# Kernel tuning notes

Measured on AMD Instinct MI355X. Metric: run time of the kernel, lower is better.

Reference implementation:

```python
import jax, jax.numpy as jnp
import numpy as np

B, N, D, H, HD = 1, 2048, 1024, 16, 64
INNER = H * HD
WINDOW_RATIO = 0.125  # docstring default in _create_window_mask


def rotate_half(x):
    # interleaved pair rotation: (x0,x1) -> (-x1,x0), per x-transformers
    pairs = x.reshape(x.shape[:-1] + (-1, 2))
    x1, x2 = pairs[..., 0], pairs[..., 1]
    return jnp.stack([-x2, x1], axis=-1).reshape(x.shape)


def apply_rope(t, freqs):
    # rotate only the first rot_dim channels, pass the rest through
    rot = freqs.shape[-1]
    t_rot, t_pass = t[..., :rot], t[..., rot:]
    t_rot = t_rot * jnp.cos(freqs) + rotate_half(t_rot) * jnp.sin(freqs)
    return jnp.concatenate([t_rot, t_pass], axis=-1)


def setup_inputs() -> dict:
    key = jax.random.key(0)
    ks = jax.random.split(key, 12)
    x = jax.random.normal(ks[0], (B, N, D), jnp.float32)
    mask = jnp.ones((B, N), dtype=bool)
    # rotary freqs of width dim_head (x-transformers style, repeated r=2)
    pos = jnp.arange(N, dtype=jnp.float32)
    inv = 1.0 / (10000.0 ** (jnp.arange(0, HD, 2, dtype=jnp.float32) / HD))
    freqs = jnp.repeat(pos[:, None] * inv[None, :], 2, axis=-1)  # [N, HD]
    s = 0.02
    Wq = jax.random.normal(ks[1], (D, INNER), jnp.float32) * s
    bq = jax.random.normal(ks[2], (INNER,), jnp.float32) * s
    Wk = jax.random.normal(ks[3], (D, INNER), jnp.float32) * s
    bk = jax.random.normal(ks[4], (INNER,), jnp.float32) * s
    Wv = jax.random.normal(ks[5], (D, INNER), jnp.float32) * s
    bv = jax.random.normal(ks[6], (INNER,), jnp.float32) * s
    Wo = jax.random.normal(ks[7], (INNER, D), jnp.float32) * s
    bo = jax.random.normal(ks[8], (D,), jnp.float32) * s
    return {"x": x, "mask": mask, "freqs": freqs, "Wq": Wq, "bq": bq,
            "Wk": Wk, "bk": bk, "Wv": Wv, "bv": bv, "Wo": Wo, "bo": bo}


def reference(x, mask, freqs, Wq, bq, Wk, bk, Wv, bv, Wo, bo):
    b, n, _ = x.shape
    q = apply_rope(x @ Wq + bq, freqs)  # q_xpos_scale = 1.0
    k = apply_rope(x @ Wk + bk, freqs)  # k_xpos_scale = 1.0
    v = x @ Wv + bv
    # [b,n,inner] -> [b,h,n,hd]
    q = q.reshape(b, n, H, HD).transpose(0, 2, 1, 3)
    k = k.reshape(b, n, H, HD).transpose(0, 2, 1, 3)
    v = v.reshape(b, n, H, HD).transpose(0, 2, 1, 3)
    scale = 1.0 / jnp.sqrt(jnp.asarray(HD, q.dtype))
    scores = jnp.einsum('bhqd,bhkd->bhqk', q, k) * scale  # computed once, reused
    # sliding-window mask: row i attends [i-ws//2, i+ws//2] inclusive
    ws = int(n * WINDOW_RATIO)
    i = jnp.arange(n)[:, None]
    j = jnp.arange(n)[None, :]
    wmask = (j >= i - ws // 2) & (j <= i + ws // 2)  # [n,n]
    keymask = mask[:, None, None, :]  # [b,1,1,n]
    NEG = jnp.asarray(-1e9, scores.dtype)
    full_p = jax.nn.softmax(jnp.where(keymask, scores, NEG), axis=-1)
    win_p = jax.nn.softmax(jnp.where(wmask[None, None] & keymask, scores, NEG), axis=-1)
    full_attn = jnp.einsum('bhqk,bhkd->bhqd', full_p, v)
    win_attn = jnp.einsum('bhqk,bhkd->bhqd', win_p, v)
    window_residual = full_attn - win_attn  # [b,h,n,hd]
    out = full_attn.transpose(0, 2, 1, 3).reshape(b, n, INNER) @ Wo + bo
    out = jnp.where(mask[..., None], out, jnp.asarray(0.0, out.dtype))
    return (out, window_residual)
```

## Files before the change

### kernel.cpp

```cpp
#include <hip/hip_runtime.h>
#include <cstdint>

#define SEQ 2048
#define DM 1024
#define NH 16
#define HD 64

typedef short s8v __attribute__((ext_vector_type(8)));
typedef float f4v __attribute__((ext_vector_type(4)));

__device__ __forceinline__ short f2bf(float x) {
  union { float f; unsigned u; } v; v.f = x;
  return (short)((v.u + 0x7fffu + ((v.u >> 16) & 1u)) >> 16);
}

__device__ __forceinline__ void load_lds16(const void* g, void* l) {
  auto gp = reinterpret_cast<const __attribute__((address_space(1))) unsigned int*>(
      reinterpret_cast<uintptr_t>(g));
  auto lp = reinterpret_cast<__attribute__((address_space(3))) unsigned int*>(
      reinterpret_cast<uintptr_t>(l));
  __builtin_amdgcn_global_load_lds(gp, lp, 16, 0, 0);
}

__global__ __launch_bounds__(256) void convert_x_kernel(const float* __restrict__ x,
                                                        short* __restrict__ xb) {
  int i = blockIdx.x * 256 + threadIdx.x;
  float4 v = ((const float4*)x)[i];
  short4 o;
  o.x = f2bf(v.x); o.y = f2bf(v.y); o.z = f2bf(v.z); o.w = f2bf(v.w);
  ((short4*)xb)[i] = o;
}

__global__ __launch_bounds__(256) void transpose_w_kernel(
    const float* __restrict__ W0, const float* __restrict__ W1,
    const float* __restrict__ W2, const float* __restrict__ W3,
    short* __restrict__ T0, short* __restrict__ T1,
    short* __restrict__ T2, short* __restrict__ T3) {
  const float* W; short* T;
  switch (blockIdx.z) {
    case 0: W = W0; T = T0; break;
    case 1: W = W1; T = T1; break;
    case 2: W = W2; T = T2; break;
    default: W = W3; T = T3; break;
  }
  __shared__ float tile[32][33];
  int tx = threadIdx.x, ty = threadIdx.y;
  int bc = blockIdx.x * 32, br = blockIdx.y * 32;
#pragma unroll
  for (int i = 0; i < 4; ++i)
    tile[ty + i * 8][tx] = W[(size_t)(br + ty + i * 8) * DM + bc + tx];
  __syncthreads();
#pragma unroll
  for (int i = 0; i < 4; ++i)
    T[(size_t)(bc + ty + i * 8) * DM + br + tx] = f2bf(tile[tx][ty + i * 8]);
}

template <int BM, int BN>
__device__ __forceinline__ void gemm_body(const short* __restrict__ A,
                                          const short* __restrict__ BT,
                                          const float* __restrict__ bias,
                                          const float* __restrict__ freqs,
                                          short* __restrict__ ob, float* __restrict__ of,
                                          int mode, short* At, short* Bt) {
  const int tid = threadIdx.x;
  const int wave = tid >> 6, lane = tid & 63;
  const int quad = lane >> 4, l16 = lane & 15;
  const int m0 = blockIdx.x * BM, n0 = blockIdx.y * BN;
  const int wm = (wave & 1) * (BM / 2), wn = (wave >> 1) * (BN / 2);
  constexpr int MI = BM / 32, NI = BN / 32;

  f4v acc[MI][NI];
  f4v zero = {0.f, 0.f, 0.f, 0.f};
#pragma unroll
  for (int i = 0; i < MI; ++i)
#pragma unroll
    for (int j = 0; j < NI; ++j) acc[i][j] = zero;

  for (int k0 = 0; k0 < DM; k0 += 32) {
#pragma unroll
    for (int i = 0; i < BM / 64; ++i) {
      int e = (tid + i * 256) * 8;
      int row = e >> 5, col = e & 31;
      load_lds16(A + (size_t)(m0 + row) * DM + k0 + col, At + (wave * 64 + i * 256) * 8);
    }
#pragma unroll
    for (int i = 0; i < BN / 64; ++i) {
      int e = (tid + i * 256) * 8;
      int row = e >> 5, col = e & 31;
      load_lds16(BT + (size_t)(n0 + row) * DM + k0 + col, Bt + (wave * 64 + i * 256) * 8);
    }
    __syncthreads();
    s8v a[MI], b[NI];
#pragma unroll
    for (int mi = 0; mi < MI; ++mi)
      a[mi] = *(const s8v*)(At + (wm + mi * 16 + l16) * 32 + quad * 8);
#pragma unroll
    for (int ni = 0; ni < NI; ++ni)
      b[ni] = *(const s8v*)(Bt + (wn + ni * 16 + l16) * 32 + quad * 8);
#pragma unroll
    for (int mi = 0; mi < MI; ++mi)
#pragma unroll
      for (int ni = 0; ni < NI; ++ni)
        acc[mi][ni] = __builtin_amdgcn_mfma_f32_16x16x32_bf16(a[mi], b[ni], acc[mi][ni], 0, 0, 0);
    __syncthreads();
  }

#pragma unroll
  for (int mi = 0; mi < MI; ++mi) {
#pragma unroll
    for (int ni = 0; ni < NI; ++ni) {
      const int col = n0 + wn + ni * 16 + l16;
      const float bv = bias[col];
      const int row0 = m0 + wm + mi * 16 + quad * 4;
      if (mode == 2) {
        short4 o;
        o.x = f2bf(acc[mi][ni][0] + bv);
        o.y = f2bf(acc[mi][ni][1] + bv);
        o.z = f2bf(acc[mi][ni][2] + bv);
        o.w = f2bf(acc[mi][ni][3] + bv);
        *(short4*)(ob + (size_t)col * SEQ + row0) = o;
      } else if (mode == 3) {
#pragma unroll
        for (int r = 0; r < 4; ++r)
          of[(size_t)(row0 + r) * DM + col] = acc[mi][ni][r] + bv;
      } else {
#pragma unroll
        for (int r = 0; r < 4; ++r) {
          const int row = row0 + r;
          float v = acc[mi][ni][r] + bv;
          if (col < HD) {
            float f = freqs[row * HD + col];
            float partner = __shfl_xor(v, 1);
            float cs = cosf(f), sn = sinf(f);
            v = v * cs + ((col & 1) ? partner : -partner) * sn;
          }
          ob[(size_t)(col >> 6) * (SEQ * HD) + (size_t)row * HD + (col & 63)] = f2bf(v);
        }
      }
    }
  }
}

__global__ __launch_bounds__(256) void gemm_qkv_kernel(
    const short* __restrict__ A, const short* __restrict__ BTq,
    const short* __restrict__ BTk, const short* __restrict__ BTv,
    const float* __restrict__ bq, const float* __restrict__ bk,
    const float* __restrict__ bv, const float* __restrict__ freqs,
    short* __restrict__ q, short* __restrict__ k, short* __restrict__ v) {
  __shared__ __align__(16) short At[64 * 32];
  __shared__ __align__(16) short Bt[128 * 32];
  const int z = blockIdx.z;
  const short* BT = z == 0 ? BTq : (z == 1 ? BTk : BTv);
  const float* bias = z == 0 ? bq : (z == 1 ? bk : bv);
  short* ob = z == 0 ? q : (z == 1 ? k : v);
  gemm_body<64, 128>(A, BT, bias, freqs, ob, nullptr, z, At, Bt);
}

__global__ __launch_bounds__(256) void gemm_o_kernel(const short* __restrict__ A,
                                                     const short* __restrict__ BT,
                                                     const float* __restrict__ bias,
                                                     float* __restrict__ of) {
  __shared__ __align__(16) short At[64 * 32];
  __shared__ __align__(16) short Bt[64 * 32];
  gemm_body<64, 64>(A, BT, bias, nullptr, nullptr, of, 3, At, Bt);
}


__device__ __forceinline__ void online_update2(const f4v sf[4], float& m, float& l,
                                               f4v O[4], short* pw, const short* vlds,
                                               int quad, int l16) {
  float mx = -3.0e38f;
#pragma unroll
  for (int nt = 0; nt < 4; ++nt)
#pragma unroll
    for (int r = 0; r < 4; ++r) mx = fmaxf(mx, sf[nt][r]);
  mx = fmaxf(mx, __shfl_xor(mx, 16));
  mx = fmaxf(mx, __shfl_xor(mx, 32));
  const float mn = fmaxf(m, mx);
  const float alpha = exp2f(m - mn);
  m = mn;
  float s = 0.f;
  unsigned pk[4][2];
#pragma unroll
  for (int nt = 0; nt < 4; ++nt) {
    float p0 = exp2f(sf[nt][0] - mn), p1 = exp2f(sf[nt][1] - mn);
    float p2 = exp2f(sf[nt][2] - mn), p3 = exp2f(sf[nt][3] - mn);
    s += (p0 + p1) + (p2 + p3);
    pk[nt][0] = ((unsigned)(unsigned short)f2bf(p1) << 16) | (unsigned short)f2bf(p0);
    pk[nt][1] = ((unsigned)(unsigned short)f2bf(p3) << 16) | (unsigned short)f2bf(p2);
  }
  s += __shfl_xor(s, 16);
  s += __shfl_xor(s, 32);
  l = l * alpha + s;
#pragma unroll
  for (int ni = 0; ni < 4; ++ni) O[ni] *= alpha;

  const int sw = l16 & 7;
#pragma unroll
  for (int nt = 0; nt < 4; ++nt) {
    uint2 w; w.x = pk[nt][0]; w.y = pk[nt][1];
    *(uint2*)(pw + l16 * 64 + (((nt * 2 + (quad >> 1)) ^ sw) << 3) + ((quad & 1) << 2)) = w;
  }
  __builtin_amdgcn_s_waitcnt(0xC07F);
  __builtin_amdgcn_wave_barrier();
  s8v bp0 = *(const s8v*)(pw + l16 * 64 + ((quad ^ sw) << 3));
  s8v bp1 = *(const s8v*)(pw + l16 * 64 + (((4 + quad) ^ sw) << 3));
#pragma unroll
  for (int ni = 0; ni < 4; ++ni) {
    const int d = ni * 16 + l16;
    const short* vr = vlds + d * 64;
    s8v va = *(const s8v*)(vr + ((quad ^ sw) << 3));
    s8v vb = *(const s8v*)(vr + (((4 + quad) ^ sw) << 3));
    O[ni] = __builtin_amdgcn_mfma_f32_16x16x32_bf16(va, bp0, O[ni], 0, 0, 0);
    O[ni] = __builtin_amdgcn_mfma_f32_16x16x32_bf16(vb, bp1, O[ni], 0, 0, 0);
  }
  __builtin_amdgcn_wave_barrier();
}

__global__ __launch_bounds__(256, 2) void attn_kernel(const short* __restrict__ qh,
                                                      const short* __restrict__ kh,
                                                      const short* __restrict__ vT,
                                                      float* __restrict__ resid,
                                                      short* __restrict__ aws) {
  __shared__ __align__(16) short Kd[2][64 * 64];
  __shared__ __align__(16) short Vd[2][64 * 64];
  __shared__ __align__(16) short Pl[4][16 * 64];
  const int tid = threadIdx.x, wave = tid >> 6, lane = tid & 63;
  const int quad = lane >> 4, l16 = lane & 15;
  const int h = blockIdx.y;
  const int q0w = blockIdx.x * 64 + wave * 16;

  const short* kbase = kh + (size_t)h * (SEQ * HD);
  const short* vbase = vT + (size_t)h * (HD * SEQ);
  short* pw = &Pl[wave][0];

  const short* qb = qh + (size_t)h * (SEQ * HD) + (size_t)(q0w + l16) * HD;
  s8v bq0 = *(const s8v*)(qb + quad * 8);
  s8v bq1 = *(const s8v*)(qb + 32 + quad * 8);

  f4v Of[4], Ow[4];
  float mf = -3.0e38f, lf = 0.f, mw = -3.0e38f, lw = 0.f;
  f4v zero = {0.f, 0.f, 0.f, 0.f};
#pragma unroll
  for (int i = 0; i < 4; ++i) { Of[i] = zero; Ow[i] = zero; }

  const float SCALE = 0.125f * 1.44269504089f;

#pragma unroll
  for (int i = 0; i < 2; ++i) {
    const int G = wave * 64 + i * 256 + lane;
    const int r = G >> 3, gc = (G & 7) ^ (r & 7);
    load_lds16(kbase + (size_t)r * HD + gc * 8, &Kd[0][(wave * 64 + i * 256) * 8]);
    load_lds16(vbase + (size_t)r * SEQ + gc * 8, &Vd[0][(wave * 64 + i * 256) * 8]);
  }
  __syncthreads();

  for (int it = 0; it < 32; ++it) {
    const int kb = it * 64, cur = it & 1;
    if (it + 1 < 32) {
      const int kb2 = kb + 64;
#pragma unroll
      for (int i = 0; i < 2; ++i) {
        const int G = wave * 64 + i * 256 + lane;
        const int r = G >> 3, gc = (G & 7) ^ (r & 7);
        load_lds16(kbase + (size_t)(kb2 + r) * HD + gc * 8,
                   &Kd[cur ^ 1][(wave * 64 + i * 256) * 8]);
        load_lds16(vbase + (size_t)r * SEQ + kb2 + gc * 8,
                   &Vd[cur ^ 1][(wave * 64 + i * 256) * 8]);
      }
    }

    f4v sf[4];
#pragma unroll
    for (int nt = 0; nt < 4; ++nt) {
      const int j = nt * 16 + l16;
      const short* kr = &Kd[cur][j * 64];
      s8v ka = *(const s8v*)(kr + ((quad ^ (j & 7)) << 3));
      s8v kc = *(const s8v*)(kr + (((4 + quad) ^ (j & 7)) << 3));
      f4v s = zero;
      s = __builtin_amdgcn_mfma_f32_16x16x32_bf16(ka, bq0, s, 0, 0, 0);
      s = __builtin_amdgcn_mfma_f32_16x16x32_bf16(kc, bq1, s, 0, 0, 0);
      sf[nt] = s * SCALE;
    }

    online_update2(sf, mf, lf, Of, pw, &Vd[cur][0], quad, l16);

    const bool band = (kb + 63 >= q0w - 128) && (kb <= q0w + 15 + 128);
    if (band) {
      f4v swv[4];
#pragma unroll
      for (int nt = 0; nt < 4; ++nt)
#pragma unroll
        for (int r = 0; r < 4; ++r) {
          const int df = (kb + nt * 16 + quad * 4 + r) - (q0w + l16);
          swv[nt][r] = (df >= -128 && df <= 128) ? sf[nt][r] : -1.0e9f;
        }
      online_update2(swv, mw, lw, Ow, pw, &Vd[cur][0], quad, l16);
    }
    __syncthreads();
  }

  const float invf = 1.0f / lf;
  const float invw = 1.0f / lw;
  const int q = q0w + l16;
  float* rbase = resid + (size_t)h * (SEQ * HD) + (size_t)q * HD;
  short* abase = aws + (size_t)q * DM + h * HD;
#pragma unroll
  for (int ni = 0; ni < 4; ++ni) {
    const int d0 = ni * 16 + quad * 4;
    f4v fullv = Of[ni] * invf;
    f4v winv = Ow[ni] * invw;
    float4 rv;
    rv.x = fullv[0] - winv[0]; rv.y = fullv[1] - winv[1];
    rv.z = fullv[2] - winv[2]; rv.w = fullv[3] - winv[3];
    *(float4*)(rbase + d0) = rv;
    short4 o;
    o.x = f2bf(fullv[0]); o.y = f2bf(fullv[1]);
    o.z = f2bf(fullv[2]); o.w = f2bf(fullv[3]);
    *(short4*)(abase + d0) = o;
  }
}

extern "C" void kernel_launch(void* const* d_in, const int* in_sizes, int n_in,
                              void* d_out, int out_size, void* d_ws, size_t ws_size,
                              hipStream_t stream) {
  const float* x     = (const float*)d_in[0];
  const float* freqs = (const float*)d_in[2];
  const float* Wq = (const float*)d_in[3];
  const float* bq = (const float*)d_in[4];
  const float* Wk = (const float*)d_in[5];
  const float* bk = (const float*)d_in[6];
  const float* Wv = (const float*)d_in[7];
  const float* bv = (const float*)d_in[8];
  const float* Wo = (const float*)d_in[9];
  const float* bo = (const float*)d_in[10];
  float* out = (float*)d_out;

  char* ws = (char*)d_ws;
  short* Xb  = (short*)(ws);
  short* WqT = (short*)(ws + ((size_t)4  << 20));
  short* WkT = (short*)(ws + ((size_t)6  << 20));
  short* WvT = (short*)(ws + ((size_t)8  << 20));
  short* WoT = (short*)(ws + ((size_t)10 << 20));
  short* qhp = (short*)(ws + ((size_t)12 << 20));
  short* khp = (short*)(ws + ((size_t)16 << 20));
  short* vTp = (short*)(ws + ((size_t)20 << 20));
  short* aws = (short*)(ws + ((size_t)24 << 20));

  convert_x_kernel<<<SEQ * DM / 4 / 256, 256, 0, stream>>>(x, Xb);
  transpose_w_kernel<<<dim3(32, 32, 4), dim3(32, 8), 0, stream>>>(
      Wq, Wk, Wv, Wo, WqT, WkT, WvT, WoT);

  gemm_qkv_kernel<<<dim3(32, 8, 3), 256, 0, stream>>>(
      Xb, WqT, WkT, WvT, bq, bk, bv, freqs, qhp, khp, vTp);

  attn_kernel<<<dim3(32, 16), 256, 0, stream>>>(
      qhp, khp, vTp, out + (size_t)SEQ * DM, aws);

  gemm_o_kernel<<<dim3(32, 16), 256, 0, stream>>>(aws, WoT, bo, out);
}
```

Before: 202.6 us.

## Retile QKV and output GEMMs, split attention KV range across wave halves

The QKV GEMM becomes one 128x128-tile kernel with a 64-wide K step and XOR-swizzled LDS, treating the three weight matrices as one contiguous transposed buffer. It also folds the softmax scale into Q at store time. The output GEMM uses a 128-wide K step with swizzled LDS. The attention kernel now runs 512 threads, where two wave groups each handle half of the key range and their online-softmax states are merged through LDS at the end, to raise parallelism and cut the per-block serial loop. In exchange, LDS use and register pressure go up, and correctness depends on WqT/WkT/WvT being laid out contiguously in the workspace.

```diff
diff --git a/kernel.cpp b/kernel.cpp
--- a/kernel.cpp
+++ b/kernel.cpp
@@ -55,116 +55,155 @@
     T[(size_t)(bc + ty + i * 8) * DM + br + tx] = f2bf(tile[tx][ty + i * 8]);
 }
 
-template <int BM, int BN>
-__device__ __forceinline__ void gemm_body(const short* __restrict__ A,
-                                          const short* __restrict__ BT,
-                                          const float* __restrict__ bias,
-                                          const float* __restrict__ freqs,
-                                          short* __restrict__ ob, float* __restrict__ of,
-                                          int mode, short* At, short* Bt) {
-  const int tid = threadIdx.x;
-  const int wave = tid >> 6, lane = tid & 63;
+__global__ __launch_bounds__(256) void gemm_qkv_kernel(
+    const short* __restrict__ A, const short* __restrict__ BT,
+    const float* __restrict__ bqp, const float* __restrict__ bkp,
+    const float* __restrict__ bvp, const float* __restrict__ freqs,
+    short* __restrict__ q, short* __restrict__ k, short* __restrict__ v) {
+  __shared__ __align__(16) short At[128 * 64];
+  __shared__ __align__(16) short Bt[128 * 64];
+  const int tid = threadIdx.x, wave = tid >> 6, lane = tid & 63;
   const int quad = lane >> 4, l16 = lane & 15;
-  const int m0 = blockIdx.x * BM, n0 = blockIdx.y * BN;
-  const int wm = (wave & 1) * (BM / 2), wn = (wave >> 1) * (BN / 2);
-  constexpr int MI = BM / 32, NI = BN / 32;
-
-  f4v acc[MI][NI];
+  const int m0 = blockIdx.x * 128;
+  const int n0g = blockIdx.y * 128;
+  const int z = blockIdx.y >> 3;
+  const int colbase = (blockIdx.y & 7) * 128;
+  const int wm = (wave & 1) * 64, wn = (wave >> 1) * 64;
+
+  f4v acc[4][4];
   f4v zero = {0.f, 0.f, 0.f, 0.f};
 #pragma unroll
-  for (int i = 0; i < MI; ++i)
-#pragma unroll
-    for (int j = 0; j < NI; ++j) acc[i][j] = zero;
-
-  for (int k0 = 0; k0 < DM; k0 += 32) {
-#pragma unroll
-    for (int i = 0; i < BM / 64; ++i) {
-      int e = (tid + i * 256) * 8;
-      int row = e >> 5, col = e & 31;
-      load_lds16(A + (size_t)(m0 + row) * DM + k0 + col, At + (wave * 64 + i * 256) * 8);
-    }
-#pragma unroll
-    for (int i = 0; i < BN / 64; ++i) {
-      int e = (tid + i * 256) * 8;
-      int row = e >> 5, col = e & 31;
-      load_lds16(BT + (size_t)(n0 + row) * DM + k0 + col, Bt + (wave * 64 + i * 256) * 8);
+  for (int i = 0; i < 4; ++i)
+#pragma unroll
+    for (int j = 0; j < 4; ++j) acc[i][j] = zero;
+
+  for (int k0 = 0; k0 < DM; k0 += 64) {
+#pragma unroll
+    for (int i = 0; i < 4; ++i) {
+      const int G = i * 256 + tid;
+      const int r = G >> 3, gc = ((G & 7) ^ (r & 7)) << 3;
+      load_lds16(A + (size_t)(m0 + r) * DM + k0 + gc, At + G * 8);
+      load_lds16(BT + (size_t)(n0g + r) * DM + k0 + gc, Bt + G * 8);
     }
     __syncthreads();
-    s8v a[MI], b[NI];
-#pragma unroll
-    for (int mi = 0; mi < MI; ++mi)
-      a[mi] = *(const s8v*)(At + (wm + mi * 16 + l16) * 32 + quad * 8);
-#pragma unroll
-    for (int ni = 0; ni < NI; ++ni)
-      b[ni] = *(const s8v*)(Bt + (wn + ni * 16 + l16) * 32 + quad * 8);
-#pragma unroll
-    for (int mi = 0; mi < MI; ++mi)
-#pragma unroll
-      for (int ni = 0; ni < NI; ++ni)
-        acc[mi][ni] = __builtin_amdgcn_mfma_f32_16x16x32_bf16(a[mi], b[ni], acc[mi][ni], 0, 0, 0);
+#pragma unroll
+    for (int kc = 0; kc < 2; ++kc) {
+      s8v a[4], b[4];
+#pragma unroll
+      for (int mi = 0; mi < 4; ++mi) {
+        const int row = wm + mi * 16 + l16;
+        a[mi] = *(const s8v*)(At + row * 64 + (((kc * 4 + quad) ^ (row & 7)) << 3));
+      }
+#pragma unroll
+      for (int ni = 0; ni < 4; ++ni) {
+        const int row = wn + ni * 16 + l16;
+        b[ni] = *(const s8v*)(Bt + row * 64 + (((kc * 4 + quad) ^ (row & 7)) << 3));
+      }
+#pragma unroll
+      for (int mi = 0; mi < 4; ++mi)
+#pragma unroll
+        for (int ni = 0; ni < 4; ++ni)
+          acc[mi][ni] = __builtin_amdgcn_mfma_f32_16x16x32_bf16(a[mi], b[ni], acc[mi][ni], 0, 0, 0);
+    }
     __syncthreads();
   }
 
-#pragma unroll
-  for (int mi = 0; mi < MI; ++mi) {
-#pragma unroll
-    for (int ni = 0; ni < NI; ++ni) {
-      const int col = n0 + wn + ni * 16 + l16;
+  const float* bias = (z == 0) ? bqp : (z == 1) ? bkp : bvp;
+  const float SCALE = 0.125f * 1.44269504089f;
+#pragma unroll
+  for (int mi = 0; mi < 4; ++mi) {
+#pragma unroll
+    for (int ni = 0; ni < 4; ++ni) {
+      const int col = colbase + wn + ni * 16 + l16;
       const float bv = bias[col];
       const int row0 = m0 + wm + mi * 16 + quad * 4;
-      if (mode == 2) {
+      if (z == 2) {
         short4 o;
         o.x = f2bf(acc[mi][ni][0] + bv);
         o.y = f2bf(acc[mi][ni][1] + bv);
         o.z = f2bf(acc[mi][ni][2] + bv);
         o.w = f2bf(acc[mi][ni][3] + bv);
-        *(short4*)(ob + (size_t)col * SEQ + row0) = o;
-      } else if (mode == 3) {
-#pragma unroll
-        for (int r = 0; r < 4; ++r)
-          of[(size_t)(row0 + r) * DM + col] = acc[mi][ni][r] + bv;
+        *(short4*)(v + (size_t)col * SEQ + row0) = o;
       } else {
+        const bool rope = (colbase + wn) == 0;
+        short* ob = (z == 0) ? q : k;
 #pragma unroll
         for (int r = 0; r < 4; ++r) {
           const int row = row0 + r;
-          float v = acc[mi][ni][r] + bv;
-          if (col < HD) {
-            float f = freqs[row * HD + col];
-            float partner = __shfl_xor(v, 1);
-            float cs = cosf(f), sn = sinf(f);
-            v = v * cs + ((col & 1) ? partner : -partner) * sn;
+          float val = acc[mi][ni][r] + bv;
+          if (rope) {
+            const float f = freqs[row * HD + col];
+            const float partner = __shfl_xor(val, 1);
+            val = val * cosf(f) + ((col & 1) ? partner : -partner) * sinf(f);
           }
-          ob[(size_t)(col >> 6) * (SEQ * HD) + (size_t)row * HD + (col & 63)] = f2bf(v);
+          if (z == 0) val *= SCALE;
+          ob[(size_t)(col >> 6) * (SEQ * HD) + (size_t)row * HD + (col & 63)] = f2bf(val);
         }
       }
     }
   }
-}
-
-__global__ __launch_bounds__(256) void gemm_qkv_kernel(
-    const short* __restrict__ A, const short* __restrict__ BTq,
-    const short* __restrict__ BTk, const short* __restrict__ BTv,
-    const float* __restrict__ bq, const float* __restrict__ bk,
-    const float* __restrict__ bv, const float* __restrict__ freqs,
-    short* __restrict__ q, short* __restrict__ k, short* __restrict__ v) {
-  __shared__ __align__(16) short At[64 * 32];
-  __shared__ __align__(16) short Bt[128 * 32];
-  const int z = blockIdx.z;
-  const short* BT = z == 0 ? BTq : (z == 1 ? BTk : BTv);
-  const float* bias = z == 0 ? bq : (z == 1 ? bk : bv);
-  short* ob = z == 0 ? q : (z == 1 ? k : v);
-  gemm_body<64, 128>(A, BT, bias, freqs, ob, nullptr, z, At, Bt);
 }
 
 __global__ __launch_bounds__(256) void gemm_o_kernel(const short* __restrict__ A,
                                                      const short* __restrict__ BT,
                                                      const float* __restrict__ bias,
                                                      float* __restrict__ of) {
-  __shared__ __align__(16) short At[64 * 32];
-  __shared__ __align__(16) short Bt[64 * 32];
-  gemm_body<64, 64>(A, BT, bias, nullptr, nullptr, of, 3, At, Bt);
-}
-
+  __shared__ __align__(16) short At[64 * 128];
+  __shared__ __align__(16) short Bt[64 * 128];
+  const int tid = threadIdx.x, wave = tid >> 6, lane = tid & 63;
+  const int quad = lane >> 4, l16 = lane & 15;
+  const int m0 = blockIdx.x * 64, n0 = blockIdx.y * 64;
+  const int wm = (wave & 1) * 32, wn = (wave >> 1) * 32;
+
+  f4v acc[2][2];
+  f4v zero = {0.f, 0.f, 0.f, 0.f};
+#pragma unroll
+  for (int i = 0; i < 2; ++i)
+#pragma unroll
+    for (int j = 0; j < 2; ++j) acc[i][j] = zero;
+
+  for (int k0 = 0; k0 < DM; k0 += 128) {
+#pragma unroll
+    for (int i = 0; i < 4; ++i) {
+      const int G = i * 256 + tid;
+      const int r = G >> 4, gc = ((G & 15) ^ (r & 15)) << 3;
+      load_lds16(A + (size_t)(m0 + r) * DM + k0 + gc, At + G * 8);
+      load_lds16(BT + (size_t)(n0 + r) * DM + k0 + gc, Bt + G * 8);
+    }
+    __syncthreads();
+#pragma unroll
+    for (int kc = 0; kc < 4; ++kc) {
+      s8v a[2], b[2];
+#pragma unroll
+      for (int mi = 0; mi < 2; ++mi) {
+        const int row = wm + mi * 16 + l16;
+        a[mi] = *(const s8v*)(At + row * 128 + (((kc * 4 + quad) ^ (row & 15)) << 3));
+      }
+#pragma unroll
+      for (int ni = 0; ni < 2; ++ni) {
+        const int row = wn + ni * 16 + l16;
+        b[ni] = *(const s8v*)(Bt + row * 128 + (((kc * 4 + quad) ^ (row & 15)) << 3));
+      }
+#pragma unroll
+      for (int mi = 0; mi < 2; ++mi)
+#pragma unroll
+        for (int ni = 0; ni < 2; ++ni)
+          acc[mi][ni] = __builtin_amdgcn_mfma_f32_16x16x32_bf16(a[mi], b[ni], acc[mi][ni], 0, 0, 0);
+    }
+    __syncthreads();
+  }
+
+#pragma unroll
+  for (int mi = 0; mi < 2; ++mi)
+#pragma unroll
+    for (int ni = 0; ni < 2; ++ni) {
+      const int col = n0 + wn + ni * 16 + l16;
+      const float bv = bias[col];
+      const int row0 = m0 + wm + mi * 16 + quad * 4;
+#pragma unroll
+      for (int r = 0; r < 4; ++r) of[(size_t)(row0 + r) * DM + col] = acc[mi][ni][r] + bv;
+    }
+}
 
 __device__ __forceinline__ void online_update2(const f4v sf[4], float& m, float& l,
                                                f4v O[4], short* pw, const short* vlds,
@@ -207,8 +246,7 @@
   s8v bp1 = *(const s8v*)(pw + l16 * 64 + (((4 + quad) ^ sw) << 3));
 #pragma unroll
   for (int ni = 0; ni < 4; ++ni) {
-    const int d = ni * 16 + l16;
-    const short* vr = vlds + d * 64;
+    const short* vr = vlds + (ni * 16 + l16) * 64;
     s8v va = *(const s8v*)(vr + ((quad ^ sw) << 3));
     s8v vb = *(const s8v*)(vr + (((4 + quad) ^ sw) << 3));
     O[ni] = __builtin_amdgcn_mfma_f32_16x16x32_bf16(va, bp0, O[ni], 0, 0, 0);
@@ -217,18 +255,19 @@
   __builtin_amdgcn_wave_barrier();
 }
 
-__global__ __launch_bounds__(256, 2) void attn_kernel(const short* __restrict__ qh,
+__global__ __launch_bounds__(512, 4) void attn_kernel(const short* __restrict__ qh,
                                                       const short* __restrict__ kh,
                                                       const short* __restrict__ vT,
                                                       float* __restrict__ resid,
                                                       short* __restrict__ aws) {
-  __shared__ __align__(16) short Kd[2][64 * 64];
-  __shared__ __align__(16) short Vd[2][64 * 64];
-  __shared__ __align__(16) short Pl[4][16 * 64];
+  __shared__ __align__(16) short Kd[2][2][64 * 64];
+  __shared__ __align__(16) short Vd[2][2][64 * 64];
+  __shared__ __align__(16) short Pl[8][16 * 64];
   const int tid = threadIdx.x, wave = tid >> 6, lane = tid & 63;
   const int quad = lane >> 4, l16 = lane & 15;
+  const int slab = wave & 3, khalf = wave >> 2;
   const int h = blockIdx.y;
-  const int q0w = blockIdx.x * 64 + wave * 16;
+  const int q0w = blockIdx.x * 64 + slab * 16;
 
   const short* kbase = kh + (size_t)h * (SEQ * HD);
   const short* vbase = vT + (size_t)h * (HD * SEQ);
@@ -244,46 +283,37 @@
 #pragma unroll
   for (int i = 0; i < 4; ++i) { Of[i] = zero; Ow[i] = zero; }
 
-  const float SCALE = 0.125f * 1.44269504089f;
-
-#pragma unroll
-  for (int i = 0; i < 2; ++i) {
-    const int G = wave * 64 + i * 256 + lane;
-    const int r = G >> 3, gc = (G & 7) ^ (r & 7);
-    load_lds16(kbase + (size_t)r * HD + gc * 8, &Kd[0][(wave * 64 + i * 256) * 8]);
-    load_lds16(vbase + (size_t)r * SEQ + gc * 8, &Vd[0][(wave * 64 + i * 256) * 8]);
-  }
+  const int sr = tid >> 3, sg = ((tid & 7) ^ (sr & 7)) << 3;
+#define STAGE(IT, BUF)                                                                  \
+  {                                                                                     \
+    load_lds16(kbase + (size_t)((IT)*64 + sr) * HD + sg, &Kd[BUF][0][tid * 8]);         \
+    load_lds16(kbase + (size_t)(((IT) + 16) * 64 + sr) * HD + sg, &Kd[BUF][1][tid * 8]);\
+    load_lds16(vbase + (size_t)sr * SEQ + (IT)*64 + sg, &Vd[BUF][0][tid * 8]);          \
+    load_lds16(vbase + (size_t)sr * SEQ + ((IT) + 16) * 64 + sg, &Vd[BUF][1][tid * 8]); \
+  }
+
+  STAGE(0, 0);
   __syncthreads();
 
-  for (int it = 0; it < 32; ++it) {
-    const int kb = it * 64, cur = it & 1;
-    if (it + 1 < 32) {
-      const int kb2 = kb + 64;
-#pragma unroll
-      for (int i = 0; i < 2; ++i) {
-        const int G = wave * 64 + i * 256 + lane;
-        const int r = G >> 3, gc = (G & 7) ^ (r & 7);
-        load_lds16(kbase + (size_t)(kb2 + r) * HD + gc * 8,
-                   &Kd[cur ^ 1][(wave * 64 + i * 256) * 8]);
-        load_lds16(vbase + (size_t)r * SEQ + kb2 + gc * 8,
-                   &Vd[cur ^ 1][(wave * 64 + i * 256) * 8]);
-      }
-    }
+  for (int it = 0; it < 16; ++it) {
+    const int cur = it & 1;
+    const int kb = (khalf * 16 + it) * 64;
+    if (it + 1 < 16) STAGE(it + 1, cur ^ 1);
 
     f4v sf[4];
 #pragma unroll
     for (int nt = 0; nt < 4; ++nt) {
       const int j = nt * 16 + l16;
-      const short* kr = &Kd[cur][j * 64];
+      const short* kr = &Kd[cur][khalf][j * 64];
       s8v ka = *(const s8v*)(kr + ((quad ^ (j & 7)) << 3));
       s8v kc = *(const s8v*)(kr + (((4 + quad) ^ (j & 7)) << 3));
       f4v s = zero;
       s = __builtin_amdgcn_mfma_f32_16x16x32_bf16(ka, bq0, s, 0, 0, 0);
       s = __builtin_amdgcn_mfma_f32_16x16x32_bf16(kc, bq1, s, 0, 0, 0);
-      sf[nt] = s * SCALE;
-    }
-
-    online_update2(sf, mf, lf, Of, pw, &Vd[cur][0], quad, l16);
+      sf[nt] = s;
+    }
+
+    online_update2(sf, mf, lf, Of, pw, &Vd[cur][khalf][0], quad, l16);
 
     const bool band = (kb + 63 >= q0w - 128) && (kb <= q0w + 15 + 128);
     if (band) {
@@ -295,29 +325,59 @@
           const int df = (kb + nt * 16 + quad * 4 + r) - (q0w + l16);
           swv[nt][r] = (df >= -128 && df <= 128) ? sf[nt][r] : -1.0e9f;
         }
-      online_update2(swv, mw, lw, Ow, pw, &Vd[cur][0], quad, l16);
+      online_update2(swv, mw, lw, Ow, pw, &Vd[cur][khalf][0], quad, l16);
     }
     __syncthreads();
   }
 
-  const float invf = 1.0f / lf;
-  const float invw = 1.0f / lw;
-  const int q = q0w + l16;
-  float* rbase = resid + (size_t)h * (SEQ * HD) + (size_t)q * HD;
-  short* abase = aws + (size_t)q * DM + h * HD;
-#pragma unroll
-  for (int ni = 0; ni < 4; ++ni) {
-    const int d0 = ni * 16 + quad * 4;
-    f4v fullv = Of[ni] * invf;
-    f4v winv = Ow[ni] * invw;
-    float4 rv;
-    rv.x = fullv[0] - winv[0]; rv.y = fullv[1] - winv[1];
-    rv.z = fullv[2] - winv[2]; rv.w = fullv[3] - winv[3];
-    *(float4*)(rbase + d0) = rv;
-    short4 o;
-    o.x = f2bf(fullv[0]); o.y = f2bf(fullv[1]);
-    o.z = f2bf(fullv[2]); o.w = f2bf(fullv[3]);
-    *(short4*)(abase + d0) = o;
+  float* OfS = (float*)&Kd[0][0][0];
+  float* OwS = (float*)&Vd[0][0][0];
+  float* mlS = (float*)&Pl[0][0];
+  if (khalf == 1) {
+#pragma unroll
+    for (int ni = 0; ni < 4; ++ni) {
+      const int d0 = ni * 16 + quad * 4;
+      *(f4v*)(OfS + (slab * 16 + l16) * 68 + d0) = Of[ni];
+      *(f4v*)(OwS + (slab * 16 + l16) * 68 + d0) = Ow[ni];
+    }
+    if (quad == 0) {
+      mlS[(slab * 4 + 0) * 16 + l16] = mf;
+      mlS[(slab * 4 + 1) * 16 + l16] = lf;
+      mlS[(slab * 4 + 2) * 16 + l16] = mw;
+      mlS[(slab * 4 + 3) * 16 + l16] = lw;
+    }
+  }
+  __syncthreads();
+  if (khalf == 0) {
+    const float mf1 = mlS[(slab * 4 + 0) * 16 + l16];
+    const float lf1 = mlS[(slab * 4 + 1) * 16 + l16];
+    const float mw1 = mlS[(slab * 4 + 2) * 16 + l16];
+    const float lw1 = mlS[(slab * 4 + 3) * 16 + l16];
+    const float m = fmaxf(mf, mf1);
+    const float a0 = exp2f(mf - m), a1 = exp2f(mf1 - m);
+    const float invf = 1.0f / (lf * a0 + lf1 * a1);
+    const float mm = fmaxf(mw, mw1);
+    const float a0w = exp2f(mw - mm), a1w = exp2f(mw1 - mm);
+    const float invw = 1.0f / (lw * a0w + lw1 * a1w);
+    const int q = q0w + l16;
+    float* rbase = resid + (size_t)h * (SEQ * HD) + (size_t)q * HD;
+    short* abase = aws + (size_t)q * DM + h * HD;
+#pragma unroll
+    for (int ni = 0; ni < 4; ++ni) {
+      const int d0 = ni * 16 + quad * 4;
+      f4v of1 = *(const f4v*)(OfS + (slab * 16 + l16) * 68 + d0);
+      f4v ow1 = *(const f4v*)(OwS + (slab * 16 + l16) * 68 + d0);
+      f4v fullv = (Of[ni] * a0 + of1 * a1) * invf;
+      f4v winv = (Ow[ni] * a0w + ow1 * a1w) * invw;
+      float4 rv;
+      rv.x = fullv[0] - winv[0]; rv.y = fullv[1] - winv[1];
+      rv.z = fullv[2] - winv[2]; rv.w = fullv[3] - winv[3];
+      *(float4*)(rbase + d0) = rv;
+      short4 o;
+      o.x = f2bf(fullv[0]); o.y = f2bf(fullv[1]);
+      o.z = f2bf(fullv[2]); o.w = f2bf(fullv[3]);
+      *(short4*)(abase + d0) = o;
+    }
   }
 }
 
@@ -351,10 +411,10 @@
   transpose_w_kernel<<<dim3(32, 32, 4), dim3(32, 8), 0, stream>>>(
       Wq, Wk, Wv, Wo, WqT, WkT, WvT, WoT);
 
-  gemm_qkv_kernel<<<dim3(32, 8, 3), 256, 0, stream>>>(
-      Xb, WqT, WkT, WvT, bq, bk, bv, freqs, qhp, khp, vTp);
-
-  attn_kernel<<<dim3(32, 16), 256, 0, stream>>>(
+  gemm_qkv_kernel<<<dim3(16, 24), 256, 0, stream>>>(
+      Xb, WqT, bq, bk, bv, freqs, qhp, khp, vTp);
+
+  attn_kernel<<<dim3(SEQ / 64, NH), 512, 0, stream>>>(
       qhp, khp, vTp, out + (size_t)SEQ * DM, aws);
 
   gemm_o_kernel<<<dim3(32, 16), 256, 0, stream>>>(aws, WoT, bo, out);
```

After: 208.8 us. 3.0% more time.
